# Kernel tuning notes

Measured on AMD Instinct MI355X. Metric: run time of the kernel, lower is better.

Reference implementation:

```python
import jax, jax.numpy as jnp
import numpy as np

S, B, V = 128, 64, 32000
EH, EO, H, O = 512, 512, 1024, 1024
THRESH = 1e-06


def _thresh(x):
    # nn.Threshold(1e-6, 0): x if x > 1e-6 else 0
    return jnp.where(x > THRESH, x, 0.0)


def setup_inputs() -> dict:
    key = jax.random.key(0)
    ks = jax.random.split(key, 12)
    ids = jax.random.randint(ks[0], (S, B), 0, V, dtype=jnp.int32)
    s = 0.02
    return {
        "ids": ids,
        "W1": jax.random.normal(ks[1], (EH, V), jnp.float32) * s,
        "b1": jax.random.normal(ks[2], (EH,), jnp.float32) * s,
        "W2": jax.random.normal(ks[3], (EO, EH), jnp.float32) * s,
        "b2": jax.random.normal(ks[4], (EO,), jnp.float32) * s,
        "W_ih": jax.random.normal(ks[5], (3 * H, EO), jnp.float32) * s,
        "b_ih": jax.random.normal(ks[6], (3 * H,), jnp.float32) * s,
        "W_hh": jax.random.normal(ks[7], (3 * H, H), jnp.float32) * s,
        "b_hh": jax.random.normal(ks[8], (3 * H,), jnp.float32) * s,
        "W_out": jax.random.normal(ks[9], (O, H), jnp.float32) * s,
        "b_out": jax.random.normal(ks[10], (O,), jnp.float32) * s,
    }


def reference(ids, W1, b1, W2, b2, W_ih, b_ih, W_hh, b_hh, W_out, b_out):
    # one_hot(ids, V) @ W1.T + b1 == exact gather of W1 columns (sum of zeros is exact)
    emb = _thresh(jnp.take(W1.T, ids, axis=0) + b1)            # [S, B, EH]
    x = _thresh(jnp.einsum('sbe,oe->sbo', emb, W2) + b2)       # [S, B, EO]
    # Precompute all input-gate projections in one GEMM
    xW = jnp.einsum('sbe,ge->sbg', x, W_ih) + b_ih             # [S, B, 3H]

    def step(h, xw):
        gh = h @ W_hh.T + b_hh                                 # [B, 3H]
        xr, xz, xn = jnp.split(xw, 3, axis=-1)
        hr, hz, hn = jnp.split(gh, 3, axis=-1)
        r = jax.nn.sigmoid(xr + hr)
        z = jax.nn.sigmoid(xz + hz)
        n = jnp.tanh(xn + r * hn)
        h_new = (1.0 - z) * n + z * h
        return h_new, None

    h0 = jnp.zeros((B, H), dtype=x.dtype)
    hT, _ = jax.lax.scan(step, h0, xW)                         # [B, H]
    # Dropout is identity in inference; final Linear
    out = hT @ W_out.T + b_out                                 # [B, O]
    return out[None]                                           # [1, B, O] (h_n layout)
```

## Files before the change

kernel.cpp:

```cpp
#include <hip/hip_runtime.h>
#include <stdint.h>
#include <stddef.h>

#define S_LEN 128
#define B_SZ  64
#define V_SZ  32000
#define EH    512
#define EO    512
#define H_SZ  1024
#define O_SZ  1024
#define G3    3072

typedef __attribute__((ext_vector_type(8))) short short8;
typedef __attribute__((ext_vector_type(4))) float floatx4;
typedef __attribute__((ext_vector_type(8))) unsigned short ushortx8;
typedef __attribute__((ext_vector_type(4))) unsigned uintx4;

__device__ __forceinline__ unsigned short f2bf(float f) {
  unsigned u = __builtin_bit_cast(unsigned, f);
  u += 0x7FFFu + ((u >> 16) & 1u);
  return (unsigned short)(u >> 16);
}
__device__ __forceinline__ float bf2f(unsigned short h) {
  unsigned u = ((unsigned)h) << 16;
  return __builtin_bit_cast(float, u);
}

__device__ __forceinline__ void gld_lds16(const void* g, void* l) {
  __builtin_amdgcn_global_load_lds((const __attribute__((address_space(1))) void*)g,
                                   (__attribute__((address_space(3))) void*)l, 16, 0, 0);
}

__global__ __launch_bounds__(256) void prep_all(const float* __restrict__ W2,
                                                const float* __restrict__ W_hh,
                                                const float* __restrict__ W_ih,
                                                const float* __restrict__ W_out,
                                                unsigned short* __restrict__ W2b,
                                                unsigned short* __restrict__ Wprep,
                                                unsigned short* __restrict__ Wihp,
                                                unsigned short* __restrict__ Woutp,
                                                unsigned* __restrict__ bar) {
  int b = blockIdx.x;
  int t = threadIdx.x;
  if (b < 256) {
    int i = b * 256 + t;
    float4 v = ((const float4*)W2)[i];
    ushort4 o;
    o.x = f2bf(v.x); o.y = f2bf(v.y); o.z = f2bf(v.z); o.w = f2bf(v.w);
    ((ushort4*)W2b)[i] = o;
    if (b == 0) bar[t] = 0;
    return;
  }
  int lane, row, k;
  const float* src;
  ushortx8* dst;
  if (b < 256 + 1536) {
    int tid = (b - 256) * 256 + t;
    lane = tid & 63;
    int c = tid >> 6;
    int cg = c / 96, r = c % 96, g = r >> 5, tt = r & 31;
    row = g * H_SZ + cg * 16 + (lane & 15);
    k   = tt * 32 + (lane >> 4) * 8;
    src = &W_hh[(size_t)row * H_SZ + k];
    dst = (ushortx8*)Wprep + tid;
  } else if (b < 256 + 1536 + 768) {
    int tid = (b - 1792) * 256 + t;
    lane = tid & 63;
    int c = tid >> 6;
    int cg = c / 48, r = c % 48, g = r >> 4, kq = r & 15;
    row = g * H_SZ + cg * 16 + (lane & 15);
    k   = kq * 32 + (lane >> 4) * 8;
    src = &W_ih[(size_t)row * EO + k];
    dst = (ushortx8*)Wihp + tid;
  } else {
    int tid = (b - 2560) * 256 + t;
    lane = tid & 63;
    int c = tid >> 6;
    int cg = c >> 5, kq = c & 31;
    row = cg * 16 + (lane & 15);
    k   = kq * 32 + (lane >> 4) * 8;
    src = &W_out[(size_t)row * H_SZ + k];
    dst = (ushortx8*)Woutp + tid;
  }
  float4 v0 = *(const float4*)src;
  float4 v1 = *(const float4*)(src + 4);
  ushortx8 o;
  o[0] = f2bf(v0.x); o[1] = f2bf(v0.y); o[2] = f2bf(v0.z); o[3] = f2bf(v0.w);
  o[4] = f2bf(v1.x); o[5] = f2bf(v1.y); o[6] = f2bf(v1.z); o[7] = f2bf(v1.w);
  *dst = o;
}

__global__ __launch_bounds__(256) void transpose_w1_bf16(const float* __restrict__ W1,
                                                         unsigned short* __restrict__ W1T) {
  __shared__ unsigned short tile[64][72];
  int t = threadIdx.x;
  int v0 = blockIdx.x * 64;
  int e0 = blockIdx.y * 64;
  for (int i = 0; i < 4; ++i) {
    int e = (t >> 4) + i * 16;
    int v = (t & 15) * 4;
    float4 w = *(const float4*)&W1[(size_t)(e0 + e) * V_SZ + v0 + v];
    tile[v + 0][e] = f2bf(w.x);
    tile[v + 1][e] = f2bf(w.y);
    tile[v + 2][e] = f2bf(w.z);
    tile[v + 3][e] = f2bf(w.w);
  }
  __syncthreads();
  for (int i = 0; i < 2; ++i) {
    int v = (t >> 3) + i * 32;
    int e = (t & 7) * 8;
    ushortx8 o;
    for (int j = 0; j < 8; ++j) o[j] = tile[v][e + j];
    *(ushortx8*)&W1T[(size_t)(v0 + v) * EH + e0 + e] = o;
  }
}

__global__ __launch_bounds__(256) void gather_emb(const int* __restrict__ ids,
                                                  const unsigned short* __restrict__ W1T,
                                                  const float* __restrict__ b1,
                                                  unsigned short* __restrict__ emb) {
  int t = threadIdx.x;
  int tok = blockIdx.x * 4 + (t >> 6);
  int lane = t & 63;
  int id = ids[tok];
  ushortx8 w = *(const ushortx8*)&W1T[(size_t)id * EH + lane * 8];
  float4 blo = *(const float4*)&b1[lane * 8];
  float4 bhi = *(const float4*)&b1[lane * 8 + 4];
  float bv[8] = {blo.x, blo.y, blo.z, blo.w, bhi.x, bhi.y, bhi.z, bhi.w};
  ushortx8 o;
  for (int j = 0; j < 8; ++j) {
    float x = bf2f(w[j]) + bv[j];
    x = (x > 1e-6f) ? x : 0.0f;
    o[j] = f2bf(x);
  }
  *(ushortx8*)&emb[(size_t)tok * EH + lane * 8] = o;
}

template <int ACT, int OUT_BF16>
__global__ __launch_bounds__(256) void gemm_bt(const unsigned short* __restrict__ A,
                                               const unsigned short* __restrict__ B,
                                               const float* __restrict__ bias,
                                               void* __restrict__ Cout,
                                               int M, int N, int K) {
  __shared__ unsigned short lA[128 * 64];
  __shared__ unsigned short lB[128 * 64];
  int t = threadIdx.x;
  int lane = t & 63;
  int wave = t >> 6;
  int bn = blockIdx.x, bm = blockIdx.y;
  int wm = (wave >> 1) * 64;
  int wn = (wave & 1) * 64;
  floatx4 acc[4][4] = {};

  int srow = t >> 3;
  int sslot = (t & 7) ^ (srow & 7);
  int scol = sslot * 8;

  const unsigned short* aptr[4];
  const unsigned short* bptr[4];
#pragma unroll
  for (int p = 0; p < 4; ++p) {
    int gra = bm * 128 + p * 32 + srow;  if (gra >= M) gra = M - 1;
    aptr[p] = A + (size_t)gra * K + scol;
    bptr[p] = B + (size_t)(bn * 128 + p * 32 + srow) * K + scol;
  }

  for (int k0 = 0; k0 < K; k0 += 64) {
    __syncthreads();
#pragma unroll
    for (int p = 0; p < 4; ++p) {
      gld_lds16(aptr[p] + k0, &lA[p * 2048 + t * 8]);
      gld_lds16(bptr[p] + k0, &lB[p * 2048 + t * 8]);
    }
    __syncthreads();
#pragma unroll
    for (int kk = 0; kk < 2; ++kk) {
      short8 af[4], bfr[4];
#pragma unroll
      for (int i = 0; i < 4; ++i) {
        int row = wm + i * 16 + (lane & 15);
        int phys = (kk * 4 + (lane >> 4)) ^ (row & 7);
        af[i] = *(const short8*)&lA[row * 64 + phys * 8];
      }
#pragma unroll
      for (int j = 0; j < 4; ++j) {
        int row = wn + j * 16 + (lane & 15);
        int phys = (kk * 4 + (lane >> 4)) ^ (row & 7);
        bfr[j] = *(const short8*)&lB[row * 64 + phys * 8];
      }
#pragma unroll
      for (int i = 0; i < 4; ++i)
#pragma unroll
        for (int j = 0; j < 4; ++j)
          acc[i][j] = __builtin_amdgcn_mfma_f32_16x16x32_bf16(af[i], bfr[j], acc[i][j], 0, 0, 0);
    }
  }

  int rowq = (lane >> 4) * 4;
  for (int j = 0; j < 4; ++j) {
    int col = bn * 128 + wn + j * 16 + (lane & 15);
    float bv = bias[col];
    for (int i = 0; i < 4; ++i) {
      int row0 = bm * 128 + wm + i * 16 + rowq;
      for (int r = 0; r < 4; ++r) {
        int row = row0 + r;
        if (row < M) {
          float v = acc[i][j][r] + bv;
          if (ACT) v = (v > 1e-6f) ? v : 0.0f;
          if (OUT_BF16) ((unsigned short*)Cout)[(size_t)row * N + col] = f2bf(v);
          else          ((float*)Cout)[(size_t)row * N + col] = v;
        }
      }
    }
  }
}

__global__ __launch_bounds__(256, 1) void gru_persist(const unsigned short* __restrict__ hprep0,
                                                      unsigned short* __restrict__ hprep1,
                                                      unsigned short* __restrict__ hbfinal,
                                                      const unsigned short* __restrict__ Wprep,
                                                      const unsigned short* __restrict__ Wihp,
                                                      const unsigned short* __restrict__ Woutp,
                                                      const float* __restrict__ b_hh,
                                                      const float* __restrict__ b_ih,
                                                      const float* __restrict__ b_out,
                                                      const unsigned short* __restrict__ x,
                                                      float* __restrict__ out,
                                                      unsigned* __restrict__ bar) {
  __shared__ unsigned short lB[96 * 512];
  __shared__ unsigned short lWih[48 * 512];
  __shared__ float lgh[3][4][256];
  __shared__ float lgxn[4][256];
  int t = threadIdx.x;
  int lane = t & 63;
  int w = t >> 6;
  int bg = blockIdx.x >> 6;
  int cg = blockIdx.x & 63;

  const unsigned short* wsrc = Wprep + (size_t)cg * 96 * 512;
  for (int i = 0; i < 24; ++i) {
    int c = w * 24 + i;
    gld_lds16(wsrc + (size_t)c * 512 + lane * 8, &lB[c * 512 + lane * 8]);
  }
  const unsigned short* wxs = Wihp + (size_t)cg * 48 * 512;
  for (int i = 0; i < 12; ++i) {
    int c = w * 12 + i;
    gld_lds16(wxs + (size_t)c * 512 + lane * 8, &lWih[c * 512 + lane * 8]);
  }

  int b_loc = t >> 4;
  int j_loc = t & 15;
  int jcol = cg * 16 + j_loc;
  int bglob = bg * 16 + b_loc;
  float brz_r = b_hh[jcol] + b_ih[jcol];
  float brz_z = b_hh[H_SZ + jcol] + b_ih[H_SZ + jcol];
  float bhn  = b_hh[2 * H_SZ + jcol];
  float bihn = b_ih[2 * H_SZ + jcol];
  int tt2 = jcol >> 5;
  int q   = (jcol >> 3) & 3;
  int jj  = jcol & 7;
  int Ls  = b_loc | (q << 4);
  size_t hw_off32 = ((((size_t)(bg * 32 + tt2) * 64 + Ls) * 8) + (jj & ~1)) >> 1;

  const unsigned short* hbufs[2] = {hprep0, hprep1};
  unsigned* barp = bar + bg * 64;
  float hmaster = 0.0f;

  const unsigned short* xbase =
      x + ((size_t)(bg * 16 + (lane & 15))) * EO + (lane >> 4) * 8 + (w * 4) * 32;

  __syncthreads();

  uintx4 xf[4];
#pragma unroll
  for (int i = 0; i < 4; ++i)
    asm volatile("global_load_dwordx4 %0, %1, off" : "=v"(xf[i]) : "v"(xbase + i * 32));

  for (int s = 0; s < S_LEN; ++s) {
    const unsigned short* hr = hbufs[s & 1];
    unsigned* hw32 = (unsigned*)hbufs[(s + 1) & 1];

    uintx4 av[8];
    if (s == 0) {
#pragma unroll
      for (int i = 0; i < 8; ++i) av[i] = (uintx4){0u, 0u, 0u, 0u};
    } else {
#pragma unroll
      for (int i = 0; i < 8; ++i) {
        int tt = w * 8 + i;
        const void* ap = hr + ((size_t)(bg * 32 + tt) * 64 + lane) * 8;
        asm volatile("global_load_dwordx4 %0, %1, off sc1" : "=v"(av[i]) : "v"(ap));
      }
    }
    asm volatile("s_waitcnt vmcnt(0)"
                 : "+v"(av[0]), "+v"(av[1]), "+v"(av[2]), "+v"(av[3]),
                   "+v"(av[4]), "+v"(av[5]), "+v"(av[6]), "+v"(av[7]),
                   "+v"(xf[0]), "+v"(xf[1]), "+v"(xf[2]), "+v"(xf[3])
                 :: "memory");

    floatx4 acc[3] = {};
    floatx4 accn = {};
#pragma unroll
    for (int i = 0; i < 8; ++i) {
      int tt = w * 8 + i;
      short8 a = __builtin_bit_cast(short8, av[i]);
#pragma unroll
      for (int g = 0; g < 3; ++g) {
        short8 bfr = *(const short8*)&lB[((g * 32 + tt) * 64 + lane) * 8];
        acc[g] = __builtin_amdgcn_mfma_f32_16x16x32_bf16(a, bfr, acc[g], 0, 0, 0);
      }
    }
#pragma unroll
    for (int i = 0; i < 4; ++i) {
      int kq = w * 4 + i;
      short8 a = __builtin_bit_cast(short8, xf[i]);
      short8 b0 = *(const short8*)&lWih[((0 * 16 + kq) * 64 + lane) * 8];
      short8 b1 = *(const short8*)&lWih[((1 * 16 + kq) * 64 + lane) * 8];
      short8 b2 = *(const short8*)&lWih[((2 * 16 + kq) * 64 + lane) * 8];
      acc[0] = __builtin_amdgcn_mfma_f32_16x16x32_bf16(a, b0, acc[0], 0, 0, 0);
      acc[1] = __builtin_amdgcn_mfma_f32_16x16x32_bf16(a, b1, acc[1], 0, 0, 0);
      accn   = __builtin_amdgcn_mfma_f32_16x16x32_bf16(a, b2, accn,   0, 0, 0);
    }

    if (s + 1 < S_LEN) {
      const unsigned short* xrow = xbase + (size_t)(s + 1) * B_SZ * EO;
#pragma unroll
      for (int i = 0; i < 4; ++i)
        asm volatile("global_load_dwordx4 %0, %1, off" : "=v"(xf[i]) : "v"(xrow + i * 32));
    }

#pragma unroll
    for (int g = 0; g < 3; ++g)
#pragma unroll
      for (int r = 0; r < 4; ++r)
        lgh[g][w][((lane >> 4) * 4 + r) * 16 + (lane & 15)] = acc[g][r];
#pragma unroll
    for (int r = 0; r < 4; ++r)
      lgxn[w][((lane >> 4) * 4 + r) * 16 + (lane & 15)] = accn[r];
    __syncthreads();

    float grs = lgh[0][0][t] + lgh[0][1][t] + lgh[0][2][t] + lgh[0][3][t] + brz_r;
    float gzs = lgh[1][0][t] + lgh[1][1][t] + lgh[1][2][t] + lgh[1][3][t] + brz_z;
    float ghn = lgh[2][0][t] + lgh[2][1][t] + lgh[2][2][t] + lgh[2][3][t] + bhn;
    float xnv = lgxn[0][t] + lgxn[1][t] + lgxn[2][t] + lgxn[3][t] + bihn;
    float rr = 1.0f / (1.0f + __expf(-grs));
    float zz = 1.0f / (1.0f + __expf(-gzs));
    float nn = tanhf(xnv + rr * ghn);
    float hnew = (1.0f - zz) * nn + zz * hmaster;
    hmaster = hnew;

    unsigned hb = (unsigned)f2bf(hnew);
    unsigned other = (unsigned)__shfl_xor((int)hb, 1);
    if ((jj & 1) == 0) {
      unsigned packed = hb | (other << 16);
      __hip_atomic_store(hw32 + hw_off32, packed,
                         __ATOMIC_RELAXED, __HIP_MEMORY_SCOPE_AGENT);
      if (s == S_LEN - 1) {
        __hip_atomic_store((unsigned*)hbfinal + (((size_t)bglob * H_SZ + jcol) >> 1),
                           packed, __ATOMIC_RELAXED, __HIP_MEMORY_SCOPE_AGENT);
      }
    }

    __syncthreads();
    if (t == 0) {
      __hip_atomic_fetch_add(barp, 1u, __ATOMIC_RELAXED, __HIP_MEMORY_SCOPE_AGENT);
      unsigned target = 64u * (unsigned)(s + 1);
      while (__hip_atomic_load(barp, __ATOMIC_RELAXED, __HIP_MEMORY_SCOPE_AGENT) < target)
        __builtin_amdgcn_s_sleep(2);
    }
    __syncthreads();
  }

  {
    const unsigned short* wos = Woutp + (size_t)cg * 32 * 512;
#pragma unroll
    for (int i = 0; i < 8; ++i) {
      int c = w * 8 + i;
      gld_lds16(wos + (size_t)c * 512 + lane * 8, &lB[c * 512 + lane * 8]);
    }
    uintx4 hv[8];
#pragma unroll
    for (int i = 0; i < 8; ++i) {
      int kq = w * 8 + i;
      const void* hp = hbfinal + (size_t)(bg * 16 + (lane & 15)) * H_SZ +
                       kq * 32 + (lane >> 4) * 8;
      asm volatile("global_load_dwordx4 %0, %1, off sc1" : "=v"(hv[i]) : "v"(hp));
    }
    __syncthreads();
    asm volatile("s_waitcnt vmcnt(0)"
                 : "+v"(hv[0]), "+v"(hv[1]), "+v"(hv[2]), "+v"(hv[3]),
                   "+v"(hv[4]), "+v"(hv[5]), "+v"(hv[6]), "+v"(hv[7])
                 :: "memory");
    floatx4 acco = {};
#pragma unroll
    for (int i = 0; i < 8; ++i) {
      int kq = w * 8 + i;
      short8 a = __builtin_bit_cast(short8, hv[i]);
      short8 bfr = *(const short8*)&lB[kq * 512 + lane * 8];
      acco = __builtin_amdgcn_mfma_f32_16x16x32_bf16(a, bfr, acco, 0, 0, 0);
    }
#pragma unroll
    for (int r = 0; r < 4; ++r)
      lgh[0][w][((lane >> 4) * 4 + r) * 16 + (lane & 15)] = acco[r];
    __syncthreads();
    float o = lgh[0][0][t] + lgh[0][1][t] + lgh[0][2][t] + lgh[0][3][t] + b_out[jcol];
    out[(size_t)bglob * O_SZ + jcol] = o;
  }
}

extern "C" void kernel_launch(void* const* d_in, const int* in_sizes, int n_in,
                              void* d_out, int out_size, void* d_ws, size_t ws_size,
                              hipStream_t stream) {
  const int*   ids   = (const int*)d_in[0];
  const float* W1    = (const float*)d_in[1];
  const float* b1    = (const float*)d_in[2];
  const float* W2    = (const float*)d_in[3];
  const float* b2    = (const float*)d_in[4];
  const float* W_ih  = (const float*)d_in[5];
  const float* b_ih  = (const float*)d_in[6];
  const float* W_hh  = (const float*)d_in[7];
  const float* b_hh  = (const float*)d_in[8];
  const float* W_out = (const float*)d_in[9];
  const float* b_out = (const float*)d_in[10];
  float* out = (float*)d_out;

  uint8_t* wsp = (uint8_t*)d_ws;
  auto alloc = [&](size_t bytes) {
    uint8_t* p = wsp;
    wsp += (bytes + 255) & ~(size_t)255;
    return p;
  };
  unsigned short* W1T   = (unsigned short*)alloc((size_t)V_SZ * EH * 2);
  unsigned short* W2b   = (unsigned short*)alloc((size_t)EO * EH * 2);
  unsigned short* Wprep = (unsigned short*)alloc((size_t)G3 * H_SZ * 2);
  unsigned short* Wihp  = (unsigned short*)alloc((size_t)G3 * EO * 2);
  unsigned short* Woutp = (unsigned short*)alloc((size_t)O_SZ * H_SZ * 2);
  unsigned short* emb   = (unsigned short*)alloc((size_t)S_LEN * B_SZ * EH * 2);
  unsigned short* x     = (unsigned short*)alloc((size_t)S_LEN * B_SZ * EO * 2);
  unsigned short* hprep0 = (unsigned short*)alloc((size_t)B_SZ * H_SZ * 2);
  unsigned short* hprep1 = (unsigned short*)alloc((size_t)B_SZ * H_SZ * 2);
  unsigned short* hbfinal = (unsigned short*)alloc((size_t)B_SZ * H_SZ * 2);
  unsigned*       bar     = (unsigned*)alloc(1024);

  prep_all<<<dim3(3072), 256, 0, stream>>>(W2, W_hh, W_ih, W_out,
                                           W2b, Wprep, Wihp, Woutp, bar);

  transpose_w1_bf16<<<dim3(V_SZ / 64, EH / 64), 256, 0, stream>>>(W1, W1T);

  gather_emb<<<dim3(S_LEN * B_SZ / 4), 256, 0, stream>>>(ids, W1T, b1, emb);

  gemm_bt<1, 1><<<dim3(EO / 128, S_LEN * B_SZ / 128), 256, 0, stream>>>(
      emb, W2b, b2, x, S_LEN * B_SZ, EO, EH);

  {
    void* args[] = {(void*)&hprep0, (void*)&hprep1, (void*)&hbfinal,
                    (void*)&Wprep, (void*)&Wihp, (void*)&Woutp,
                    (void*)&b_hh, (void*)&b_ih, (void*)&b_out,
                    (void*)&x, (void*)&out, (void*)&bar};
    hipLaunchCooperativeKernel((const void*)gru_persist, dim3(256), dim3(256),
                               args, 0, stream);
  }
}
```

Baseline: 591.6 us.

## Fuse W1 transpose, embedding gather and W2 GEMM into persistent GRU kernel

The separate transpose, gather and embedding-GEMM kernels are folded into the cooperative GRU kernel as three phases separated by grid-wide atomic barriers. Intermediate writes use agent-scope atomic stores and reads use sc1 loads so data stays coherent across blocks without kernel boundaries. This removes three kernel launches and their inter-kernel gaps. In exchange, those phases now run on only 256 blocks at one block per CU instead of wide grids, and the GEMM A-operand path loses the direct global-to-LDS load.

```diff
diff --git a/kernel.cpp b/kernel.cpp
--- a/kernel.cpp
+++ b/kernel.cpp
@@ -15,6 +15,7 @@
 typedef __attribute__((ext_vector_type(4))) float floatx4;
 typedef __attribute__((ext_vector_type(8))) unsigned short ushortx8;
 typedef __attribute__((ext_vector_type(4))) unsigned uintx4;
+typedef __attribute__((ext_vector_type(2))) unsigned long long ulonglongx2;
 
 __device__ __forceinline__ unsigned short f2bf(float f) {
   unsigned u = __builtin_bit_cast(unsigned, f);
@@ -29,6 +30,12 @@
 __device__ __forceinline__ void gld_lds16(const void* g, void* l) {
   __builtin_amdgcn_global_load_lds((const __attribute__((address_space(1))) void*)g,
                                    (__attribute__((address_space(3))) void*)l, 16, 0, 0);
+}
+__device__ __forceinline__ void st8_agent(void* p, unsigned long long v) {
+  __hip_atomic_store((unsigned long long*)p, v, __ATOMIC_RELAXED, __HIP_MEMORY_SCOPE_AGENT);
+}
+__device__ __forceinline__ void st4_agent(void* p, unsigned v) {
+  __hip_atomic_store((unsigned*)p, v, __ATOMIC_RELAXED, __HIP_MEMORY_SCOPE_AGENT);
 }
 
 __global__ __launch_bounds__(256) void prep_all(const float* __restrict__ W2,
@@ -90,132 +97,15 @@
   *dst = o;
 }
 
-__global__ __launch_bounds__(256) void transpose_w1_bf16(const float* __restrict__ W1,
-                                                         unsigned short* __restrict__ W1T) {
-  __shared__ unsigned short tile[64][72];
-  int t = threadIdx.x;
-  int v0 = blockIdx.x * 64;
-  int e0 = blockIdx.y * 64;
-  for (int i = 0; i < 4; ++i) {
-    int e = (t >> 4) + i * 16;
-    int v = (t & 15) * 4;
-    float4 w = *(const float4*)&W1[(size_t)(e0 + e) * V_SZ + v0 + v];
-    tile[v + 0][e] = f2bf(w.x);
-    tile[v + 1][e] = f2bf(w.y);
-    tile[v + 2][e] = f2bf(w.z);
-    tile[v + 3][e] = f2bf(w.w);
-  }
-  __syncthreads();
-  for (int i = 0; i < 2; ++i) {
-    int v = (t >> 3) + i * 32;
-    int e = (t & 7) * 8;
-    ushortx8 o;
-    for (int j = 0; j < 8; ++j) o[j] = tile[v][e + j];
-    *(ushortx8*)&W1T[(size_t)(v0 + v) * EH + e0 + e] = o;
-  }
-}
-
-__global__ __launch_bounds__(256) void gather_emb(const int* __restrict__ ids,
-                                                  const unsigned short* __restrict__ W1T,
-                                                  const float* __restrict__ b1,
-                                                  unsigned short* __restrict__ emb) {
-  int t = threadIdx.x;
-  int tok = blockIdx.x * 4 + (t >> 6);
-  int lane = t & 63;
-  int id = ids[tok];
-  ushortx8 w = *(const ushortx8*)&W1T[(size_t)id * EH + lane * 8];
-  float4 blo = *(const float4*)&b1[lane * 8];
-  float4 bhi = *(const float4*)&b1[lane * 8 + 4];
-  float bv[8] = {blo.x, blo.y, blo.z, blo.w, bhi.x, bhi.y, bhi.z, bhi.w};
-  ushortx8 o;
-  for (int j = 0; j < 8; ++j) {
-    float x = bf2f(w[j]) + bv[j];
-    x = (x > 1e-6f) ? x : 0.0f;
-    o[j] = f2bf(x);
-  }
-  *(ushortx8*)&emb[(size_t)tok * EH + lane * 8] = o;
-}
-
-template <int ACT, int OUT_BF16>
-__global__ __launch_bounds__(256) void gemm_bt(const unsigned short* __restrict__ A,
-                                               const unsigned short* __restrict__ B,
-                                               const float* __restrict__ bias,
-                                               void* __restrict__ Cout,
-                                               int M, int N, int K) {
-  __shared__ unsigned short lA[128 * 64];
-  __shared__ unsigned short lB[128 * 64];
-  int t = threadIdx.x;
-  int lane = t & 63;
-  int wave = t >> 6;
-  int bn = blockIdx.x, bm = blockIdx.y;
-  int wm = (wave >> 1) * 64;
-  int wn = (wave & 1) * 64;
-  floatx4 acc[4][4] = {};
-
-  int srow = t >> 3;
-  int sslot = (t & 7) ^ (srow & 7);
-  int scol = sslot * 8;
-
-  const unsigned short* aptr[4];
-  const unsigned short* bptr[4];
-#pragma unroll
-  for (int p = 0; p < 4; ++p) {
-    int gra = bm * 128 + p * 32 + srow;  if (gra >= M) gra = M - 1;
-    aptr[p] = A + (size_t)gra * K + scol;
-    bptr[p] = B + (size_t)(bn * 128 + p * 32 + srow) * K + scol;
-  }
-
-  for (int k0 = 0; k0 < K; k0 += 64) {
-    __syncthreads();
-#pragma unroll
-    for (int p = 0; p < 4; ++p) {
-      gld_lds16(aptr[p] + k0, &lA[p * 2048 + t * 8]);
-      gld_lds16(bptr[p] + k0, &lB[p * 2048 + t * 8]);
-    }
-    __syncthreads();
-#pragma unroll
-    for (int kk = 0; kk < 2; ++kk) {
-      short8 af[4], bfr[4];
-#pragma unroll
-      for (int i = 0; i < 4; ++i) {
-        int row = wm + i * 16 + (lane & 15);
-        int phys = (kk * 4 + (lane >> 4)) ^ (row & 7);
-        af[i] = *(const short8*)&lA[row * 64 + phys * 8];
-      }
-#pragma unroll
-      for (int j = 0; j < 4; ++j) {
-        int row = wn + j * 16 + (lane & 15);
-        int phys = (kk * 4 + (lane >> 4)) ^ (row & 7);
-        bfr[j] = *(const short8*)&lB[row * 64 + phys * 8];
-      }
-#pragma unroll
-      for (int i = 0; i < 4; ++i)
-#pragma unroll
-        for (int j = 0; j < 4; ++j)
-          acc[i][j] = __builtin_amdgcn_mfma_f32_16x16x32_bf16(af[i], bfr[j], acc[i][j], 0, 0, 0);
-    }
-  }
-
-  int rowq = (lane >> 4) * 4;
-  for (int j = 0; j < 4; ++j) {
-    int col = bn * 128 + wn + j * 16 + (lane & 15);
-    float bv = bias[col];
-    for (int i = 0; i < 4; ++i) {
-      int row0 = bm * 128 + wm + i * 16 + rowq;
-      for (int r = 0; r < 4; ++r) {
-        int row = row0 + r;
-        if (row < M) {
-          float v = acc[i][j][r] + bv;
-          if (ACT) v = (v > 1e-6f) ? v : 0.0f;
-          if (OUT_BF16) ((unsigned short*)Cout)[(size_t)row * N + col] = f2bf(v);
-          else          ((float*)Cout)[(size_t)row * N + col] = v;
-        }
-      }
-    }
-  }
-}
-
-__global__ __launch_bounds__(256, 1) void gru_persist(const unsigned short* __restrict__ hprep0,
+__global__ __launch_bounds__(256, 1) void gru_persist(const int* __restrict__ ids,
+                                                      const float* __restrict__ W1,
+                                                      const float* __restrict__ b1,
+                                                      const unsigned short* __restrict__ W2b,
+                                                      const float* __restrict__ b2,
+                                                      unsigned short* __restrict__ W1T,
+                                                      unsigned short* __restrict__ emb,
+                                                      unsigned short* __restrict__ x,
+                                                      const unsigned short* __restrict__ hprep0,
                                                       unsigned short* __restrict__ hprep1,
                                                       unsigned short* __restrict__ hbfinal,
                                                       const unsigned short* __restrict__ Wprep,
@@ -224,7 +114,6 @@
                                                       const float* __restrict__ b_hh,
                                                       const float* __restrict__ b_ih,
                                                       const float* __restrict__ b_out,
-                                                      const unsigned short* __restrict__ x,
                                                       float* __restrict__ out,
                                                       unsigned* __restrict__ bar) {
   __shared__ unsigned short lB[96 * 512];
@@ -234,8 +123,159 @@
   int t = threadIdx.x;
   int lane = t & 63;
   int w = t >> 6;
-  int bg = blockIdx.x >> 6;
-  int cg = blockIdx.x & 63;
+  int bid = blockIdx.x;
+  int bg = bid >> 6;
+  int cg = bid & 63;
+
+  unsigned* gctr = bar + 32;
+  auto grid_sync = [&](unsigned target) {
+    __syncthreads();
+    if (t == 0) {
+      __hip_atomic_fetch_add(gctr, 1u, __ATOMIC_RELAXED, __HIP_MEMORY_SCOPE_AGENT);
+      while (__hip_atomic_load(gctr, __ATOMIC_RELAXED, __HIP_MEMORY_SCOPE_AGENT) < target)
+        __builtin_amdgcn_s_sleep(2);
+    }
+    __syncthreads();
+  };
+
+  {
+    unsigned short (*tile)[72] = (unsigned short (*)[72])lB;
+    for (int tile_id = bid; tile_id < 4000; tile_id += 256) {
+      int v0 = (tile_id % 500) * 64;
+      int e0 = (tile_id / 500) * 64;
+      __syncthreads();
+      for (int i = 0; i < 4; ++i) {
+        int e = (t >> 4) + i * 16;
+        int v = (t & 15) * 4;
+        float4 wv = *(const float4*)&W1[(size_t)(e0 + e) * V_SZ + v0 + v];
+        tile[v + 0][e] = f2bf(wv.x);
+        tile[v + 1][e] = f2bf(wv.y);
+        tile[v + 2][e] = f2bf(wv.z);
+        tile[v + 3][e] = f2bf(wv.w);
+      }
+      __syncthreads();
+      for (int i = 0; i < 2; ++i) {
+        int v = (t >> 3) + i * 32;
+        int e = (t & 7) * 8;
+        ushortx8 o;
+        for (int j = 0; j < 8; ++j) o[j] = tile[v][e + j];
+        ulonglongx2 p = __builtin_bit_cast(ulonglongx2, o);
+        unsigned long long* dst = (unsigned long long*)&W1T[(size_t)(v0 + v) * EH + e0 + e];
+        st8_agent(dst, p[0]);
+        st8_agent(dst + 1, p[1]);
+      }
+    }
+  }
+  grid_sync(256);
+
+  {
+    float4 blo = *(const float4*)&b1[lane * 8];
+    float4 bhi = *(const float4*)&b1[lane * 8 + 4];
+    float bv[8] = {blo.x, blo.y, blo.z, blo.w, bhi.x, bhi.y, bhi.z, bhi.w};
+    int tok0 = bid * 4 + w;
+    uintx4 wv[8];
+#pragma unroll
+    for (int it = 0; it < 8; ++it) {
+      int id = ids[tok0 + it * 1024];
+      const void* ap = &W1T[(size_t)id * EH + lane * 8];
+      asm volatile("global_load_dwordx4 %0, %1, off sc1" : "=v"(wv[it]) : "v"(ap));
+    }
+    asm volatile("s_waitcnt vmcnt(0)"
+                 : "+v"(wv[0]), "+v"(wv[1]), "+v"(wv[2]), "+v"(wv[3]),
+                   "+v"(wv[4]), "+v"(wv[5]), "+v"(wv[6]), "+v"(wv[7])
+                 :: "memory");
+#pragma unroll
+    for (int it = 0; it < 8; ++it) {
+      ushortx8 w8 = __builtin_bit_cast(ushortx8, wv[it]);
+      ushortx8 o;
+#pragma unroll
+      for (int j = 0; j < 8; ++j) {
+        float xv = bf2f(w8[j]) + bv[j];
+        xv = (xv > 1e-6f) ? xv : 0.0f;
+        o[j] = f2bf(xv);
+      }
+      ulonglongx2 p = __builtin_bit_cast(ulonglongx2, o);
+      unsigned long long* dst =
+          (unsigned long long*)&emb[(size_t)(tok0 + it * 1024) * EH + lane * 8];
+      st8_agent(dst, p[0]);
+      st8_agent(dst + 1, p[1]);
+    }
+  }
+  grid_sync(512);
+
+  {
+    unsigned short* xlA = lB;
+    unsigned short* xlB = lB + 128 * 64;
+    int bn = bid >> 6;
+    int bm = bid & 63;
+    int wm = (w >> 1) * 64;
+    int wn = (w & 1) * 64;
+    floatx4 acc[4][4] = {};
+    int srow = t >> 3;
+    int sslot = (t & 7) ^ (srow & 7);
+    int scol = sslot * 8;
+    const unsigned short* aptr[4];
+    const unsigned short* bptr[4];
+#pragma unroll
+    for (int p = 0; p < 4; ++p) {
+      aptr[p] = emb + (size_t)(bm * 128 + p * 32 + srow) * EH + scol;
+      bptr[p] = W2b + (size_t)(bn * 128 + p * 32 + srow) * EH + scol;
+    }
+    for (int k0 = 0; k0 < EH; k0 += 64) {
+      __syncthreads();
+      uintx4 sa[4];
+#pragma unroll
+      for (int p = 0; p < 4; ++p) {
+        asm volatile("global_load_dwordx4 %0, %1, off sc1" : "=v"(sa[p]) : "v"(aptr[p] + k0));
+        gld_lds16(bptr[p] + k0, &xlB[p * 2048 + t * 8]);
+      }
+      asm volatile("s_waitcnt vmcnt(0)"
+                   : "+v"(sa[0]), "+v"(sa[1]), "+v"(sa[2]), "+v"(sa[3]) :: "memory");
+#pragma unroll
+      for (int p = 0; p < 4; ++p)
+        *(uintx4*)&xlA[p * 2048 + t * 8] = sa[p];
+      __syncthreads();
+#pragma unroll
+      for (int kk = 0; kk < 2; ++kk) {
+        short8 af[4], bfr[4];
+#pragma unroll
+        for (int i = 0; i < 4; ++i) {
+          int row = wm + i * 16 + (lane & 15);
+          int phys = (kk * 4 + (lane >> 4)) ^ (row & 7);
+          af[i] = *(const short8*)&xlA[row * 64 + phys * 8];
+        }
+#pragma unroll
+        for (int j = 0; j < 4; ++j) {
+          int row = wn + j * 16 + (lane & 15);
+          int phys = (kk * 4 + (lane >> 4)) ^ (row & 7);
+          bfr[j] = *(const short8*)&xlB[row * 64 + phys * 8];
+        }
+#pragma unroll
+        for (int i = 0; i < 4; ++i)
+#pragma unroll
+          for (int j = 0; j < 4; ++j)
+            acc[i][j] = __builtin_amdgcn_mfma_f32_16x16x32_bf16(af[i], bfr[j], acc[i][j], 0, 0, 0);
+      }
+    }
+    int rowq = (lane >> 4) * 4;
+    for (int j = 0; j < 4; ++j) {
+      int col = bn * 128 + wn + j * 16 + (lane & 15);
+      float bv = b2[col];
+      for (int i = 0; i < 4; ++i) {
+        int row0 = bm * 128 + wm + i * 16 + rowq;
+        for (int r = 0; r < 4; ++r) {
+          int row = row0 + r;
+          float v = acc[i][j][r] + bv;
+          v = (v > 1e-6f) ? v : 0.0f;
+          unsigned hb = (unsigned)f2bf(v);
+          unsigned other = (unsigned)__shfl_xor((int)hb, 1);
+          if ((lane & 1) == 0)
+            st4_agent((unsigned*)x + (((size_t)row * EO + col) >> 1), hb | (other << 16));
+        }
+      }
+    }
+  }
+  grid_sync(768);
 
   const unsigned short* wsrc = Wprep + (size_t)cg * 96 * 512;
   for (int i = 0; i < 24; ++i) {
@@ -274,7 +314,7 @@
   uintx4 xf[4];
 #pragma unroll
   for (int i = 0; i < 4; ++i)
-    asm volatile("global_load_dwordx4 %0, %1, off" : "=v"(xf[i]) : "v"(xbase + i * 32));
+    asm volatile("global_load_dwordx4 %0, %1, off sc1" : "=v"(xf[i]) : "v"(xbase + i * 32));
 
   for (int s = 0; s < S_LEN; ++s) {
     const unsigned short* hr = hbufs[s & 1];
@@ -315,18 +355,18 @@
       int kq = w * 4 + i;
       short8 a = __builtin_bit_cast(short8, xf[i]);
       short8 b0 = *(const short8*)&lWih[((0 * 16 + kq) * 64 + lane) * 8];
-      short8 b1 = *(const short8*)&lWih[((1 * 16 + kq) * 64 + lane) * 8];
-      short8 b2 = *(const short8*)&lWih[((2 * 16 + kq) * 64 + lane) * 8];
+      short8 b1f = *(const short8*)&lWih[((1 * 16 + kq) * 64 + lane) * 8];
+      short8 b2f = *(const short8*)&lWih[((2 * 16 + kq) * 64 + lane) * 8];
       acc[0] = __builtin_amdgcn_mfma_f32_16x16x32_bf16(a, b0, acc[0], 0, 0, 0);
-      acc[1] = __builtin_amdgcn_mfma_f32_16x16x32_bf16(a, b1, acc[1], 0, 0, 0);
-      accn   = __builtin_amdgcn_mfma_f32_16x16x32_bf16(a, b2, accn,   0, 0, 0);
+      acc[1] = __builtin_amdgcn_mfma_f32_16x16x32_bf16(a, b1f, acc[1], 0, 0, 0);
+      accn   = __builtin_amdgcn_mfma_f32_16x16x32_bf16(a, b2f, accn,   0, 0, 0);
     }
 
     if (s + 1 < S_LEN) {
       const unsigned short* xrow = xbase + (size_t)(s + 1) * B_SZ * EO;
 #pragma unroll
       for (int i = 0; i < 4; ++i)
-        asm volatile("global_load_dwordx4 %0, %1, off" : "=v"(xf[i]) : "v"(xrow + i * 32));
+        asm volatile("global_load_dwordx4 %0, %1, off sc1" : "=v"(xf[i]) : "v"(xrow + i * 32));
     }
 
 #pragma unroll
@@ -353,12 +393,9 @@
     unsigned other = (unsigned)__shfl_xor((int)hb, 1);
     if ((jj & 1) == 0) {
       unsigned packed = hb | (other << 16);
-      __hip_atomic_store(hw32 + hw_off32, packed,
-                         __ATOMIC_RELAXED, __HIP_MEMORY_SCOPE_AGENT);
-      if (s == S_LEN - 1) {
-        __hip_atomic_store((unsigned*)hbfinal + (((size_t)bglob * H_SZ + jcol) >> 1),
-                           packed, __ATOMIC_RELAXED, __HIP_MEMORY_SCOPE_AGENT);
-      }
+      st4_agent(hw32 + hw_off32, packed);
+      if (s == S_LEN - 1)
+        st4_agent((unsigned*)hbfinal + (((size_t)bglob * H_SZ + jcol) >> 1), packed);
     }
 
     __syncthreads();
@@ -445,18 +482,13 @@
   prep_all<<<dim3(3072), 256, 0, stream>>>(W2, W_hh, W_ih, W_out,
                                            W2b, Wprep, Wihp, Woutp, bar);
 
-  transpose_w1_bf16<<<dim3(V_SZ / 64, EH / 64), 256, 0, stream>>>(W1, W1T);
-
-  gather_emb<<<dim3(S_LEN * B_SZ / 4), 256, 0, stream>>>(ids, W1T, b1, emb);
-
-  gemm_bt<1, 1><<<dim3(EO / 128, S_LEN * B_SZ / 128), 256, 0, stream>>>(
-      emb, W2b, b2, x, S_LEN * B_SZ, EO, EH);
-
   {
-    void* args[] = {(void*)&hprep0, (void*)&hprep1, (void*)&hbfinal,
+    void* args[] = {(void*)&ids, (void*)&W1, (void*)&b1, (void*)&W2b, (void*)&b2,
+                    (void*)&W1T, (void*)&emb, (void*)&x,
+                    (void*)&hprep0, (void*)&hprep1, (void*)&hbfinal,
                     (void*)&Wprep, (void*)&Wihp, (void*)&Woutp,
                     (void*)&b_hh, (void*)&b_ih, (void*)&b_out,
-                    (void*)&x, (void*)&out, (void*)&bar};
+                    (void*)&out, (void*)&bar};
     hipLaunchCooperativeKernel((const void*)gru_persist, dim3(256), dim3(256),
                                args, 0, stream);
   }
```

After: 629.1 us. 6.3% more time.

## Fuse W1 transpose into prep kernel and embedding gather into x GEMM

Applied to the files above, without the earlier changes.

Merges the W1 transpose/bf16 conversion into the weight prep kernel as extra blocks, and folds the embedding gather plus bias and threshold directly into the A-tile load of the W2 GEMM. This removes two kernel launches and the emb intermediate buffer round trip through global memory. In exchange the GEMM A-operand now goes through registers instead of direct global-to-LDS loads, which may add latency in the GEMM loop.

```diff
diff --git a/kernel.cpp b/kernel.cpp
--- a/kernel.cpp
+++ b/kernel.cpp
@@ -31,17 +31,43 @@
                                    (__attribute__((address_space(3))) void*)l, 16, 0, 0);
 }
 
-__global__ __launch_bounds__(256) void prep_all(const float* __restrict__ W2,
-                                                const float* __restrict__ W_hh,
-                                                const float* __restrict__ W_ih,
-                                                const float* __restrict__ W_out,
-                                                unsigned short* __restrict__ W2b,
-                                                unsigned short* __restrict__ Wprep,
-                                                unsigned short* __restrict__ Wihp,
-                                                unsigned short* __restrict__ Woutp,
-                                                unsigned* __restrict__ bar) {
+__global__ __launch_bounds__(256) void prep_transpose(const float* __restrict__ W1,
+                                                      const float* __restrict__ W2,
+                                                      const float* __restrict__ W_hh,
+                                                      const float* __restrict__ W_ih,
+                                                      const float* __restrict__ W_out,
+                                                      unsigned short* __restrict__ W1T,
+                                                      unsigned short* __restrict__ W2b,
+                                                      unsigned short* __restrict__ Wprep,
+                                                      unsigned short* __restrict__ Wihp,
+                                                      unsigned short* __restrict__ Woutp,
+                                                      unsigned* __restrict__ bar) {
+  __shared__ unsigned short tile[64][72];
   int b = blockIdx.x;
   int t = threadIdx.x;
+  if (b < 4000) {
+    int v0 = (b % 500) * 64;
+    int e0 = (b / 500) * 64;
+    for (int i = 0; i < 4; ++i) {
+      int e = (t >> 4) + i * 16;
+      int v = (t & 15) * 4;
+      float4 w = *(const float4*)&W1[(size_t)(e0 + e) * V_SZ + v0 + v];
+      tile[v + 0][e] = f2bf(w.x);
+      tile[v + 1][e] = f2bf(w.y);
+      tile[v + 2][e] = f2bf(w.z);
+      tile[v + 3][e] = f2bf(w.w);
+    }
+    __syncthreads();
+    for (int i = 0; i < 2; ++i) {
+      int v = (t >> 3) + i * 32;
+      int e = (t & 7) * 8;
+      ushortx8 o;
+      for (int j = 0; j < 8; ++j) o[j] = tile[v][e + j];
+      *(ushortx8*)&W1T[(size_t)(v0 + v) * EH + e0 + e] = o;
+    }
+    return;
+  }
+  b -= 4000;
   if (b < 256) {
     int i = b * 256 + t;
     float4 v = ((const float4*)W2)[i];
@@ -90,58 +116,12 @@
   *dst = o;
 }
 
-__global__ __launch_bounds__(256) void transpose_w1_bf16(const float* __restrict__ W1,
-                                                         unsigned short* __restrict__ W1T) {
-  __shared__ unsigned short tile[64][72];
-  int t = threadIdx.x;
-  int v0 = blockIdx.x * 64;
-  int e0 = blockIdx.y * 64;
-  for (int i = 0; i < 4; ++i) {
-    int e = (t >> 4) + i * 16;
-    int v = (t & 15) * 4;
-    float4 w = *(const float4*)&W1[(size_t)(e0 + e) * V_SZ + v0 + v];
-    tile[v + 0][e] = f2bf(w.x);
-    tile[v + 1][e] = f2bf(w.y);
-    tile[v + 2][e] = f2bf(w.z);
-    tile[v + 3][e] = f2bf(w.w);
-  }
-  __syncthreads();
-  for (int i = 0; i < 2; ++i) {
-    int v = (t >> 3) + i * 32;
-    int e = (t & 7) * 8;
-    ushortx8 o;
-    for (int j = 0; j < 8; ++j) o[j] = tile[v][e + j];
-    *(ushortx8*)&W1T[(size_t)(v0 + v) * EH + e0 + e] = o;
-  }
-}
-
-__global__ __launch_bounds__(256) void gather_emb(const int* __restrict__ ids,
-                                                  const unsigned short* __restrict__ W1T,
-                                                  const float* __restrict__ b1,
-                                                  unsigned short* __restrict__ emb) {
-  int t = threadIdx.x;
-  int tok = blockIdx.x * 4 + (t >> 6);
-  int lane = t & 63;
-  int id = ids[tok];
-  ushortx8 w = *(const ushortx8*)&W1T[(size_t)id * EH + lane * 8];
-  float4 blo = *(const float4*)&b1[lane * 8];
-  float4 bhi = *(const float4*)&b1[lane * 8 + 4];
-  float bv[8] = {blo.x, blo.y, blo.z, blo.w, bhi.x, bhi.y, bhi.z, bhi.w};
-  ushortx8 o;
-  for (int j = 0; j < 8; ++j) {
-    float x = bf2f(w[j]) + bv[j];
-    x = (x > 1e-6f) ? x : 0.0f;
-    o[j] = f2bf(x);
-  }
-  *(ushortx8*)&emb[(size_t)tok * EH + lane * 8] = o;
-}
-
-template <int ACT, int OUT_BF16>
-__global__ __launch_bounds__(256) void gemm_bt(const unsigned short* __restrict__ A,
-                                               const unsigned short* __restrict__ B,
-                                               const float* __restrict__ bias,
-                                               void* __restrict__ Cout,
-                                               int M, int N, int K) {
+__global__ __launch_bounds__(256) void gemm_x(const int* __restrict__ ids,
+                                              const unsigned short* __restrict__ W1T,
+                                              const float* __restrict__ b1,
+                                              const unsigned short* __restrict__ W2b,
+                                              const float* __restrict__ b2,
+                                              unsigned short* __restrict__ x) {
   __shared__ unsigned short lA[128 * 64];
   __shared__ unsigned short lB[128 * 64];
   int t = threadIdx.x;
@@ -156,21 +136,36 @@
   int sslot = (t & 7) ^ (srow & 7);
   int scol = sslot * 8;
 
-  const unsigned short* aptr[4];
+  int aid[4];
   const unsigned short* bptr[4];
 #pragma unroll
   for (int p = 0; p < 4; ++p) {
-    int gra = bm * 128 + p * 32 + srow;  if (gra >= M) gra = M - 1;
-    aptr[p] = A + (size_t)gra * K + scol;
-    bptr[p] = B + (size_t)(bn * 128 + p * 32 + srow) * K + scol;
-  }
-
-  for (int k0 = 0; k0 < K; k0 += 64) {
-    __syncthreads();
+    aid[p] = ids[bm * 128 + p * 32 + srow];
+    bptr[p] = W2b + (size_t)(bn * 128 + p * 32 + srow) * EH + scol;
+  }
+
+  for (int k0 = 0; k0 < EH; k0 += 64) {
+    __syncthreads();
+    uintx4 va[4];
 #pragma unroll
     for (int p = 0; p < 4; ++p) {
-      gld_lds16(aptr[p] + k0, &lA[p * 2048 + t * 8]);
       gld_lds16(bptr[p] + k0, &lB[p * 2048 + t * 8]);
+      va[p] = *(const uintx4*)&W1T[(size_t)aid[p] * EH + k0 + scol];
+    }
+    float4 b1lo = *(const float4*)&b1[k0 + scol];
+    float4 b1hi = *(const float4*)&b1[k0 + scol + 4];
+    float bv[8] = {b1lo.x, b1lo.y, b1lo.z, b1lo.w, b1hi.x, b1hi.y, b1hi.z, b1hi.w};
+#pragma unroll
+    for (int p = 0; p < 4; ++p) {
+      ushortx8 w8 = __builtin_bit_cast(ushortx8, va[p]);
+      ushortx8 o;
+#pragma unroll
+      for (int j = 0; j < 8; ++j) {
+        float v = bf2f(w8[j]) + bv[j];
+        v = (v > 1e-6f) ? v : 0.0f;
+        o[j] = f2bf(v);
+      }
+      *(ushortx8*)&lA[p * 2048 + t * 8] = o;
     }
     __syncthreads();
 #pragma unroll
@@ -199,17 +194,14 @@
   int rowq = (lane >> 4) * 4;
   for (int j = 0; j < 4; ++j) {
     int col = bn * 128 + wn + j * 16 + (lane & 15);
-    float bv = bias[col];
+    float bv = b2[col];
     for (int i = 0; i < 4; ++i) {
       int row0 = bm * 128 + wm + i * 16 + rowq;
       for (int r = 0; r < 4; ++r) {
         int row = row0 + r;
-        if (row < M) {
-          float v = acc[i][j][r] + bv;
-          if (ACT) v = (v > 1e-6f) ? v : 0.0f;
-          if (OUT_BF16) ((unsigned short*)Cout)[(size_t)row * N + col] = f2bf(v);
-          else          ((float*)Cout)[(size_t)row * N + col] = v;
-        }
+        float v = acc[i][j][r] + bv;
+        v = (v > 1e-6f) ? v : 0.0f;
+        x[(size_t)row * EO + col] = f2bf(v);
       }
     }
   }
@@ -315,11 +307,11 @@
       int kq = w * 4 + i;
       short8 a = __builtin_bit_cast(short8, xf[i]);
       short8 b0 = *(const short8*)&lWih[((0 * 16 + kq) * 64 + lane) * 8];
-      short8 b1 = *(const short8*)&lWih[((1 * 16 + kq) * 64 + lane) * 8];
-      short8 b2 = *(const short8*)&lWih[((2 * 16 + kq) * 64 + lane) * 8];
+      short8 b1f = *(const short8*)&lWih[((1 * 16 + kq) * 64 + lane) * 8];
+      short8 b2f = *(const short8*)&lWih[((2 * 16 + kq) * 64 + lane) * 8];
       acc[0] = __builtin_amdgcn_mfma_f32_16x16x32_bf16(a, b0, acc[0], 0, 0, 0);
-      acc[1] = __builtin_amdgcn_mfma_f32_16x16x32_bf16(a, b1, acc[1], 0, 0, 0);
-      accn   = __builtin_amdgcn_mfma_f32_16x16x32_bf16(a, b2, accn,   0, 0, 0);
+      acc[1] = __builtin_amdgcn_mfma_f32_16x16x32_bf16(a, b1f, acc[1], 0, 0, 0);
+      accn   = __builtin_amdgcn_mfma_f32_16x16x32_bf16(a, b2f, accn,   0, 0, 0);
     }
 
     if (s + 1 < S_LEN) {
@@ -435,22 +427,17 @@
   unsigned short* Wprep = (unsigned short*)alloc((size_t)G3 * H_SZ * 2);
   unsigned short* Wihp  = (unsigned short*)alloc((size_t)G3 * EO * 2);
   unsigned short* Woutp = (unsigned short*)alloc((size_t)O_SZ * H_SZ * 2);
-  unsigned short* emb   = (unsigned short*)alloc((size_t)S_LEN * B_SZ * EH * 2);
   unsigned short* x     = (unsigned short*)alloc((size_t)S_LEN * B_SZ * EO * 2);
   unsigned short* hprep0 = (unsigned short*)alloc((size_t)B_SZ * H_SZ * 2);
   unsigned short* hprep1 = (unsigned short*)alloc((size_t)B_SZ * H_SZ * 2);
   unsigned short* hbfinal = (unsigned short*)alloc((size_t)B_SZ * H_SZ * 2);
   unsigned*       bar     = (unsigned*)alloc(1024);
 
-  prep_all<<<dim3(3072), 256, 0, stream>>>(W2, W_hh, W_ih, W_out,
-                                           W2b, Wprep, Wihp, Woutp, bar);
-
-  transpose_w1_bf16<<<dim3(V_SZ / 64, EH / 64), 256, 0, stream>>>(W1, W1T);
-
-  gather_emb<<<dim3(S_LEN * B_SZ / 4), 256, 0, stream>>>(ids, W1T, b1, emb);
-
-  gemm_bt<1, 1><<<dim3(EO / 128, S_LEN * B_SZ / 128), 256, 0, stream>>>(
-      emb, W2b, b2, x, S_LEN * B_SZ, EO, EH);
+  prep_transpose<<<dim3(4000 + 3072), 256, 0, stream>>>(
+      W1, W2, W_hh, W_ih, W_out, W1T, W2b, Wprep, Wihp, Woutp, bar);
+
+  gemm_x<<<dim3(EO / 128, S_LEN * B_SZ / 128), 256, 0, stream>>>(
+      ids, W1T, b1, W2b, b2, x);
 
   {
     void* args[] = {(void*)&hprep0, (void*)&hprep1, (void*)&hbfinal,
```

Measured after the change: 573.7 us (median of 2 runs). -3.0%, faster.
